# Kernel tuning notes

Hardware: AMD Instinct MI355X
Metric: run time of the kernel (lower is better)

Reference implementation:

```python
import jax, jax.numpy as jnp
import numpy as np

POWER = 2.0
EPS = jnp.float32(np.finfo(np.float32).eps)


def setup_inputs() -> dict:
    key = jax.random.key(0)
    k1, k2, k3 = jax.random.split(key, 3)
    B, P, S = 2, 131072, 512
    station_coords = jax.random.uniform(k1, (B, S, 2), dtype=jnp.float32)
    station_values = jax.random.normal(k2, (B, S), dtype=jnp.float32)
    grid_points = jax.random.uniform(k3, (B, P, 2), dtype=jnp.float32)
    return {
        "station_coords": station_coords,
        "station_values": station_values,
        "grid_points": grid_points,
    }


def reference(station_coords, station_values, grid_points):
    # grid_points: (B, P, 2); station_coords: (B, S, 2)
    diff = grid_points[:, :, None, :] - station_coords[:, None, :, :]  # (B, P, S, 2)
    distances = jnp.sqrt(jnp.sum(diff * diff, axis=-1))                # (B, P, S)
    distances = jnp.where(distances == 0, EPS, distances)
    weights = 1.0 / distances ** POWER                                  # (B, P, S)
    weights_sum = jnp.sum(weights, axis=-1)                             # (B, P)
    interpolated = jnp.sum(weights * station_values[:, None, :], axis=-1) / weights_sum
    return interpolated  # (B, P)
```

## Files before the change

kernel.cpp:

```cpp
#include <hip/hip_runtime.h>
#include <hip/hip_bf16.h>


#define BLOCK 256

__global__ __launch_bounds__(BLOCK) void idw_kernel(
    const float* __restrict__ station_coords,
    const float* __restrict__ station_values,
    const float* __restrict__ grid_points,
    float* __restrict__ out,
    int P, int S) {

    const int b = blockIdx.y;
    const int p = blockIdx.x * BLOCK + threadIdx.x;
    if (p >= P) return;

    const float2* __restrict__ sc2 = (const float2*)(station_coords) + (size_t)b * S;
    const float*  __restrict__ svb = station_values + (size_t)b * S;

    const float2 g = ((const float2*)grid_points)[(size_t)b * P + p];
    const float gx = g.x, gy = g.y;

    constexpr float EPS  = 1.1920928955078125e-07f;
    constexpr float EPS2 = EPS * EPS;

    float wsum = 0.0f;
    float vsum = 0.0f;

#pragma unroll 8
    for (int s = 0; s < S; ++s) {
        const float2 sxy = sc2[s];
        const float  v   = svb[s];
        const float dx = gx - sxy.x;
        const float dy = gy - sxy.y;
        float d2 = fmaf(dx, dx, dy * dy);
        d2 = fmaxf(d2, EPS2);
        const float w = __builtin_amdgcn_rcpf(d2);
        wsum += w;
        vsum = fmaf(w, v, vsum);
    }

    out[(size_t)b * P + p] = vsum / wsum;
}

extern "C" void kernel_launch(void* const* d_in, const int* in_sizes, int n_in,
                              void* d_out, int out_size, void* d_ws, size_t ws_size,
                              hipStream_t stream) {
    const float* station_coords = (const float*)d_in[0];
    const float* station_values = (const float*)d_in[1];
    const float* grid_points    = (const float*)d_in[2];
    float* out = (float*)d_out;

    const int B = 2;
    const int S = in_sizes[1] / B;
    const int P = out_size / B;

    dim3 grid((P + BLOCK - 1) / BLOCK, B);
    dim3 block(BLOCK);
    idw_kernel<<<grid, block, 0, stream>>>(station_coords, station_values,
                                           grid_points, out, P, S);
}
```

Measured before the change: 87.89 us.

## Stage stations in LDS and pair reciprocals to halve rcp count

Loads station coords and values into shared memory as packed float4 per block, replacing per-thread global (scalar/broadcast) loads. The inner loop processes two stations at once and computes 1/a + 1/b as (a+b)/(ab) with a single reciprocal, cutting transcendental ops in half. This risks overflow/underflow when the product of squared distances is extreme (e.g., EPS2 squared underflows), and assumes S is even and at most 512.

```diff
diff --git a/kernel.cpp b/kernel.cpp
--- a/kernel.cpp
+++ b/kernel.cpp
@@ -3,6 +3,7 @@
 
 
 #define BLOCK 256
+#define S_MAX 512
 
 __global__ __launch_bounds__(BLOCK) void idw_kernel(
     const float* __restrict__ station_coords,
@@ -11,12 +12,20 @@
     float* __restrict__ out,
     int P, int S) {
 
+    __shared__ float4 st[S_MAX];
+
     const int b = blockIdx.y;
+    const float2* __restrict__ sc2 = (const float2*)(station_coords) + (size_t)b * S;
+    const float*  __restrict__ svb = station_values + (size_t)b * S;
+
+    for (int i = threadIdx.x; i < S; i += BLOCK) {
+        const float2 c = sc2[i];
+        st[i] = make_float4(c.x, c.y, svb[i], 0.0f);
+    }
+    __syncthreads();
+
     const int p = blockIdx.x * BLOCK + threadIdx.x;
     if (p >= P) return;
-
-    const float2* __restrict__ sc2 = (const float2*)(station_coords) + (size_t)b * S;
-    const float*  __restrict__ svb = station_values + (size_t)b * S;
 
     const float2 g = ((const float2*)grid_points)[(size_t)b * P + p];
     const float gx = g.x, gy = g.y;
@@ -28,16 +37,24 @@
     float vsum = 0.0f;
 
 #pragma unroll 8
-    for (int s = 0; s < S; ++s) {
-        const float2 sxy = sc2[s];
-        const float  v   = svb[s];
-        const float dx = gx - sxy.x;
-        const float dy = gy - sxy.y;
-        float d2 = fmaf(dx, dx, dy * dy);
-        d2 = fmaxf(d2, EPS2);
-        const float w = __builtin_amdgcn_rcpf(d2);
-        wsum += w;
-        vsum = fmaf(w, v, vsum);
+    for (int s = 0; s < S; s += 2) {
+        const float4 s0 = st[s];
+        const float4 s1 = st[s + 1];
+
+        const float dx0 = gx - s0.x, dy0 = gy - s0.y;
+        float a = fmaf(dx0, dx0, dy0 * dy0);
+        a = fmaxf(a, EPS2);
+
+        const float dx1 = gx - s1.x, dy1 = gy - s1.y;
+        float bq = fmaf(dx1, dx1, dy1 * dy1);
+        bq = fmaxf(bq, EPS2);
+
+        const float ab = a * bq;
+        const float r  = __builtin_amdgcn_rcpf(ab);
+        wsum = fmaf(a + bq, r, wsum);
+        const float m    = s0.z * bq;
+        const float vnum = fmaf(s1.z, a, m);
+        vsum = fmaf(vnum, r, vsum);
     }
 
     out[(size_t)b * P + p] = vsum / wsum;
```

Measured after the change: 92.26 us. +5.0%, slower.
